# Performance work log

Hardware: AMD Instinct MI355X
Metric: run time of the kernel (lower is better)

Reference implementation:

```python
import jax, jax.numpy as jnp
import numpy as np

N_NODES = 50000
NEG_SLOPE_ATT = 0.2   # PyG GATConv default LeakyReLU slope for attention logits
NEG_SLOPE_ACT = 0.01  # nn.LeakyReLU default between layers


def _add_self_loops(src, dst, n):
    loop = jnp.arange(n, dtype=src.dtype)
    return jnp.concatenate([src, loop]), jnp.concatenate([dst, loop])


def gat_conv(x, W, a_src, a_dst, b, src, dst, n):
    # x: [N, Cin], W: [Cin, Cout], a_src/a_dst: [Cout], b: [Cout]
    h = x @ W                                   # [N, Cout]
    alpha_src = h @ a_src                       # [N]
    alpha_dst = h @ a_dst                       # [N]
    e = jax.nn.leaky_relu(alpha_src[src] + alpha_dst[dst], NEG_SLOPE_ATT)  # [E]
    # segment softmax over incoming edges of each dst node
    m = jax.ops.segment_max(e, dst, num_segments=n)      # [N]
    ex = jnp.exp(e - m[dst])                              # [E]
    s = jax.ops.segment_sum(ex, dst, num_segments=n)      # [N] (>0: self-loops)
    alpha = ex / s[dst]                                   # [E]
    out = jax.ops.segment_sum(h[src] * alpha[:, None], dst, num_segments=n)
    return out + b


def setup_inputs() -> dict:
    key = jax.random.key(0)
    ks = jax.random.split(key, 20)
    n, e = N_NODES, 800000
    cin, h1, h2, cout = 64, 128, 64, 32
    d = {
        "x": jax.random.normal(ks[0], (n, cin), jnp.float32),
        "edge_index": jax.random.randint(ks[1], (2, e), 0, n, jnp.int64),
    }
    dims = [(cin, h1), (h1, h2), (h2, h1), (h1, cout)]
    for i, (ci, co) in enumerate(dims, 1):
        g = 1.0 / np.sqrt(ci)
        d[f"W{i}"] = jax.random.normal(ks[2 + 4 * i], (ci, co), jnp.float32) * g
        d[f"a{i}s"] = jax.random.normal(ks[3 + 4 * i], (co,), jnp.float32) * 0.1
        d[f"a{i}d"] = jax.random.normal(ks[4 + 4 * i], (co,), jnp.float32) * 0.1
        d[f"b{i}"] = jnp.zeros((co,), jnp.float32)
    return d


def reference(x, edge_index, W1, a1s, a1d, b1, W2, a2s, a2d, b2,
              W3, a3s, a3d, b3, W4, a4s, a4d, b4):
    n = x.shape[0]
    src, dst = _add_self_loops(edge_index[0], edge_index[1], n)
    act = lambda t: jax.nn.leaky_relu(t, NEG_SLOPE_ACT)
    h = act(gat_conv(x, W1, a1s, a1d, b1, src, dst, n))
    # dropout is identity at inference
    h = act(gat_conv(h, W2, a2s, a2d, b2, src, dst, n))
    h = act(gat_conv(h, W3, a3s, a3d, b3, src, dst, n))
    return gat_conv(h, W4, a4s, a4d, b4, src, dst, n)
```

## Files before the change

kernel.cpp:

```cpp
#include <hip/hip_runtime.h>
#include <hip/hip_fp16.h>

#define NEG_ATT 0.2f


__global__ __launch_bounds__(256) void setup_k(int* cnt, int N, int NB,
                                               const float* __restrict__ W1, const float* __restrict__ a1s,
                                               const float* __restrict__ a1d, const float* __restrict__ W3,
                                               const float* __restrict__ a3s, const float* __restrict__ a3d,
                                               float* __restrict__ wa ) {
    int b = blockIdx.x;
    if (b < NB) {
        int i = b * 256 + threadIdx.x;
        if (i < N) cnt[i] = 0;
    } else {
        int t = threadIdx.x;
        int ci = t & 63;
        int which = t >> 6;
        const float* W = (which < 2) ? W1 : W3;
        const float* a = (which == 0) ? a1s : (which == 1) ? a1d : (which == 2) ? a3s : a3d;
        float s = 0.f;
        for (int co = 0; co < 128; ++co) s += W[ci * 128 + co] * a[co];
        wa[t] = s;
    }
}


__global__ __launch_bounds__(256) void scatter_gemv_k(const int* __restrict__ src, const int* __restrict__ dst,
                                                      int* cnt, unsigned short* __restrict__ col,
                                                      int E, int step, int SB, int iters4,
                                                      const float* __restrict__ X,
                                                      const float* __restrict__ was, const float* __restrict__ wad,
                                                      float* __restrict__ as_, float* __restrict__ ad_,
                                                      __half* __restrict__ x16, int N) {
    if (blockIdx.x < SB) {
        int part = blockIdx.x & 7;
        int lo = part * step, hi = lo + step;
        int tg = (blockIdx.x >> 3) * 256 + threadIdx.x;
        int stride = (SB >> 3) * 256;
        const int4* dst4 = (const int4*)dst;
        int E4 = E >> 2;
        for (int it = 0; it < iters4; ++it) {
            int i4 = tg + it * stride;
            if (i4 < E4) {
                int4 d4 = dst4[i4];
                int base = i4 << 2;
                if (d4.x >= lo && d4.x < hi) { int s = atomicAdd(&cnt[d4.x], 1); col[(d4.x << 6) + s] = (unsigned short)src[base]; }
                if (d4.y >= lo && d4.y < hi) { int s = atomicAdd(&cnt[d4.y], 1); col[(d4.y << 6) + s] = (unsigned short)src[base + 1]; }
                if (d4.z >= lo && d4.z < hi) { int s = atomicAdd(&cnt[d4.z], 1); col[(d4.z << 6) + s] = (unsigned short)src[base + 2]; }
                if (d4.w >= lo && d4.w < hi) { int s = atomicAdd(&cnt[d4.w], 1); col[(d4.w << 6) + s] = (unsigned short)src[base + 3]; }
            }
        }
        for (int i = (E & ~3) + tg; i < E; i += stride) {
            int dd = dst[i];
            if (dd >= lo && dd < hi) { int s = atomicAdd(&cnt[dd], 1); col[(dd << 6) + s] = (unsigned short)src[i]; }
        }
    } else {
        int wid  = ((blockIdx.x - SB) * 256 + threadIdx.x) >> 6;
        int lane = threadIdx.x & 63;
        if (wid >= N) return;
        float xv = X[(size_t)wid * 64 + lane];
        x16[(size_t)wid * 64 + lane] = __float2half(xv);
        float s1 = xv * was[lane];
        float s2 = xv * wad[lane];
        #pragma unroll
        for (int off = 32; off; off >>= 1) {
            s1 += __shfl_xor(s1, off);
            s2 += __shfl_xor(s2, off);
        }
        if (lane == 0) { as_[wid] = s1; ad_[wid] = s2; }
    }
}


__global__ __launch_bounds__(256) void gemm_wide_k(const __half* __restrict__ X16, const float* __restrict__ W,
                                                   const float* __restrict__ bias, __half* __restrict__ H16, int N) {
    __shared__ float Xs[128][68];
    __shared__ float Ws[64][128];
    int tid  = threadIdx.x;
    int row0 = blockIdx.x * 128;

    for (int i = tid; i < 2048; i += 256)
        *(float4*)&((float*)Ws)[i * 4] = *(const float4*)&W[i * 4];
    for (int i = tid; i < 2048; i += 256) {
        int r = i >> 4, k4 = i & 15;
        int gr = row0 + r;
        float4 v = {0.f, 0.f, 0.f, 0.f};
        if (gr < N) {
            uint2 pk = *(const uint2*)&X16[(size_t)gr * 64 + k4 * 4];
            float2 f0 = __half22float2(*(__half2*)&pk.x);
            float2 f1 = __half22float2(*(__half2*)&pk.y);
            v = make_float4(f0.x, f0.y, f1.x, f1.y);
        }
        *(float4*)&Xs[r][k4 * 4] = v;
    }
    __syncthreads();

    int ct = tid & 15;
    int rt = tid >> 4;
    float acc[8][8] = {};
    for (int k = 0; k < 64; k += 4) {
        float4 w0a = *(float4*)&Ws[k][ct * 8],     w0b = *(float4*)&Ws[k][ct * 8 + 4];
        float4 w1a = *(float4*)&Ws[k + 1][ct * 8], w1b = *(float4*)&Ws[k + 1][ct * 8 + 4];
        float4 w2a = *(float4*)&Ws[k + 2][ct * 8], w2b = *(float4*)&Ws[k + 2][ct * 8 + 4];
        float4 w3a = *(float4*)&Ws[k + 3][ct * 8], w3b = *(float4*)&Ws[k + 3][ct * 8 + 4];
        #pragma unroll
        for (int i = 0; i < 8; ++i) {
            float4 xv = *(float4*)&Xs[rt + 16 * i][k];
            acc[i][0] += xv.x * w0a.x + xv.y * w1a.x + xv.z * w2a.x + xv.w * w3a.x;
            acc[i][1] += xv.x * w0a.y + xv.y * w1a.y + xv.z * w2a.y + xv.w * w3a.y;
            acc[i][2] += xv.x * w0a.z + xv.y * w1a.z + xv.z * w2a.z + xv.w * w3a.z;
            acc[i][3] += xv.x * w0a.w + xv.y * w1a.w + xv.z * w2a.w + xv.w * w3a.w;
            acc[i][4] += xv.x * w0b.x + xv.y * w1b.x + xv.z * w2b.x + xv.w * w3b.x;
            acc[i][5] += xv.x * w0b.y + xv.y * w1b.y + xv.z * w2b.y + xv.w * w3b.y;
            acc[i][6] += xv.x * w0b.z + xv.y * w1b.z + xv.z * w2b.z + xv.w * w3b.z;
            acc[i][7] += xv.x * w0b.w + xv.y * w1b.w + xv.z * w2b.w + xv.w * w3b.w;
        }
    }

    float bv[8];
    #pragma unroll
    for (int j = 0; j < 8; ++j) bv[j] = bias[ct * 8 + j];

    #pragma unroll
    for (int i = 0; i < 8; ++i) {
        int gr = row0 + rt + 16 * i;
        if (gr < N) {
            float o[8];
            #pragma unroll
            for (int j = 0; j < 8; ++j) {
                float v = acc[i][j] + bv[j];
                o[j] = v > 0.f ? v : 0.01f * v;
            }
            __half2 h0 = __floats2half2_rn(o[0], o[1]);
            __half2 h1 = __floats2half2_rn(o[2], o[3]);
            __half2 h2 = __floats2half2_rn(o[4], o[5]);
            __half2 h3 = __floats2half2_rn(o[6], o[7]);
            uint4 pk = { *(unsigned*)&h0, *(unsigned*)&h1, *(unsigned*)&h2, *(unsigned*)&h3 };
            *(uint4*)&H16[(size_t)gr * 128 + ct * 8] = pk;
        }
    }
}


template <int CIN, int COUT>
__global__ __launch_bounds__(256) void gemm_k(const __half* __restrict__ X16, const float* __restrict__ W,
                                              const float* __restrict__ a_s, const float* __restrict__ a_d,
                                              __half* __restrict__ Hh, float* __restrict__ as_,
                                              float* __restrict__ ad_, int N) {
    constexpr int RB  = (CIN == 128 && COUT == 64) ? 32 : 64;
    constexpr int NCT = COUT / 4;
    constexpr int NRT = 256 / NCT;
    constexpr int RT  = RB / NRT;
    constexpr int XP  = CIN + 4;
    __shared__ float Xs[RB][XP];
    __shared__ float Ws[CIN][COUT];
    int tid  = threadIdx.x;
    int row0 = blockIdx.x * RB;

    for (int i = tid; i < CIN * COUT / 4; i += 256)
        *(float4*)&((float*)Ws)[i * 4] = *(const float4*)&W[i * 4];
    for (int i = tid; i < RB * CIN / 4; i += 256) {
        int r = i / (CIN / 4), k4 = i % (CIN / 4);
        int gr = row0 + r;
        float4 v = {0.f, 0.f, 0.f, 0.f};
        if (gr < N) {
            uint2 pk = *(const uint2*)&X16[(size_t)gr * CIN + k4 * 4];
            float2 f0 = __half22float2(*(__half2*)&pk.x);
            float2 f1 = __half22float2(*(__half2*)&pk.y);
            v = make_float4(f0.x, f0.y, f1.x, f1.y);
        }
        *(float4*)&Xs[r][k4 * 4] = v;
    }
    __syncthreads();

    int ct = tid % NCT;
    int rt = tid / NCT;
    float acc[RT][4] = {};
    for (int k = 0; k < CIN; k += 4) {
        float4 w0 = *(float4*)&Ws[k][ct * 4];
        float4 w1 = *(float4*)&Ws[k + 1][ct * 4];
        float4 w2 = *(float4*)&Ws[k + 2][ct * 4];
        float4 w3 = *(float4*)&Ws[k + 3][ct * 4];
        #pragma unroll
        for (int i = 0; i < RT; ++i) {
            float4 xv = *(float4*)&Xs[rt + i * NRT][k];
            acc[i][0] += xv.x * w0.x + xv.y * w1.x + xv.z * w2.x + xv.w * w3.x;
            acc[i][1] += xv.x * w0.y + xv.y * w1.y + xv.z * w2.y + xv.w * w3.y;
            acc[i][2] += xv.x * w0.z + xv.y * w1.z + xv.z * w2.z + xv.w * w3.z;
            acc[i][3] += xv.x * w0.w + xv.y * w1.w + xv.z * w2.w + xv.w * w3.w;
        }
    }

    float asv[4], adv[4];
    #pragma unroll
    for (int j = 0; j < 4; ++j) { asv[j] = a_s[ct * 4 + j]; adv[j] = a_d[ct * 4 + j]; }

    #pragma unroll
    for (int i = 0; i < RT; ++i) {
        int gr = row0 + rt + i * NRT;
        float s1 = acc[i][0] * asv[0] + acc[i][1] * asv[1] + acc[i][2] * asv[2] + acc[i][3] * asv[3];
        float s2 = acc[i][0] * adv[0] + acc[i][1] * adv[1] + acc[i][2] * adv[2] + acc[i][3] * adv[3];
        #pragma unroll
        for (int off = 1; off < NCT; off <<= 1) {
            s1 += __shfl_xor(s1, off);
            s2 += __shfl_xor(s2, off);
        }
        if (gr < N) {
            __half2 p0 = __floats2half2_rn(acc[i][0], acc[i][1]);
            __half2 p1 = __floats2half2_rn(acc[i][2], acc[i][3]);
            uint2 pk = { *(unsigned*)&p0, *(unsigned*)&p1 };
            *(uint2*)&Hh[(size_t)gr * COUT + ct * 4] = pk;
            if (ct == 0) { as_[gr] = s1; ad_[gr] = s2; }
        }
    }
}


template <int C, int MODE>
__global__ __launch_bounds__(256) void agg_k(const __half* __restrict__ Hg, const float* __restrict__ as_,
                                             const float* __restrict__ ad_, const int* __restrict__ deg,
                                             const unsigned short* __restrict__ col, const float* __restrict__ bias,
                                             const float* __restrict__ was, const float* __restrict__ wad,
                                             float* __restrict__ outf, __half* __restrict__ outh,
                                             float* __restrict__ oas, float* __restrict__ oad, int N) {
    __shared__ int2 sw[4][64];
    int wid  = (blockIdx.x * 256 + threadIdx.x) >> 6;
    int lane = threadIdx.x & 63;
    int wvi  = threadIdx.x >> 6;
    if (wid >= N) return;
    float adi = ad_[wid];
    int dg = deg[wid];
    float a0 = 0.f, a1 = 0.f, b0 = 0.f, b1 = 0.f;
    const int sub  = lane >> 5, c32 = lane & 31;
    const int quad = lane >> 4, c16 = lane & 15;

    int s_l = 0; float w_l = 0.f;
    if (lane < dg) {
        s_l = col[(wid << 6) + lane];
        float e = as_[s_l] + adi;
        e = e > 0.f ? e : NEG_ATT * e;
        w_l = __expf(e);
    }
    sw[wvi][lane] = make_int2(s_l, __float_as_int(w_l));

    float es = as_[wid] + adi;
    es = es > 0.f ? es : NEG_ATT * es;
    float ws = __expf(es);
    float denom = w_l + ((lane == 0) ? ws : 0.f);
    if (C == 64) {
        if (!sub) {
            float2 f = __half22float2(*(const __half2*)&Hg[((size_t)wid << 6) + 2 * c32]);
            a0 += ws * f.x; a1 += ws * f.y;
        }
    } else {
        if (!quad) {
            float2 f = __half22float2(*(const __half2*)&Hg[((size_t)wid << 5) + 2 * c16]);
            a0 += ws * f.x; a1 += ws * f.y;
        }
    }

    auto g64 = [&](int j, auto NEhalf) {
        constexpr int M = decltype(NEhalf)::value;
        float2 hv[M]; float wv[M];
        #pragma unroll
        for (int u = 0; u < M; ++u) {
            int2 p = sw[wvi][j + 2 * u + sub];
            wv[u] = __int_as_float(p.y);
            hv[u] = __half22float2(*(const __half2*)&Hg[((size_t)p.x << 6) + 2 * c32]);
        }
        #pragma unroll
        for (int u = 0; u < M; ++u) {
            if (u & 1) { b0 += wv[u] * hv[u].x; b1 += wv[u] * hv[u].y; }
            else       { a0 += wv[u] * hv[u].x; a1 += wv[u] * hv[u].y; }
        }
    };
    auto g32 = [&](int j, auto NEq) {
        constexpr int M = decltype(NEq)::value;
        float2 hv[M]; float wv[M];
        #pragma unroll
        for (int u = 0; u < M; ++u) {
            int2 p = sw[wvi][j + 4 * u + quad];
            wv[u] = __int_as_float(p.y);
            hv[u] = __half22float2(*(const __half2*)&Hg[((size_t)p.x << 5) + 2 * c16]);
        }
        #pragma unroll
        for (int u = 0; u < M; ++u) {
            if (u & 1) { b0 += wv[u] * hv[u].x; b1 += wv[u] * hv[u].y; }
            else       { a0 += wv[u] * hv[u].x; a1 += wv[u] * hv[u].y; }
        }
    };

    if (C == 64) {
        if (dg <= 8)       g64(0, std::integral_constant<int, 4>{});
        else if (dg <= 16) g64(0, std::integral_constant<int, 8>{});
        else if (dg <= 32) g64(0, std::integral_constant<int, 16>{});
        else { g64(0, std::integral_constant<int, 16>{}); g64(32, std::integral_constant<int, 16>{}); }
    } else {
        if (dg <= 16)      g32(0, std::integral_constant<int, 4>{});
        else if (dg <= 32) g32(0, std::integral_constant<int, 8>{});
        else { g32(0, std::integral_constant<int, 8>{}); g32(32, std::integral_constant<int, 8>{}); }
    }

    float f0 = a0 + b0, f1 = a1 + b1;
    if (C == 32) { f0 += __shfl_xor(f0, 16); f1 += __shfl_xor(f1, 16); }
    f0 += __shfl_xor(f0, 32); f1 += __shfl_xor(f1, 32);
    #pragma unroll
    for (int off = 32; off; off >>= 1) denom += __shfl_xor(denom, off);

    float inv = 1.f / denom;
    float v0 = f0 * inv, v1 = f1 * inv;

    if (MODE == 0) {
        if (!sub) {
            __half2 p = __floats2half2_rn(v0, v1);
            *(__half2*)&outh[((size_t)wid << 6) + 2 * c32] = p;
        }
    } else if (MODE == 1) {
        float2 bb = *(const float2*)&bias[2 * c32];
        v0 += bb.x; v1 += bb.y;
        v0 = v0 > 0.f ? v0 : 0.01f * v0;
        v1 = v1 > 0.f ? v1 : 0.01f * v1;
        if (!sub) {
            __half2 p = __floats2half2_rn(v0, v1);
            *(__half2*)&outh[((size_t)wid << 6) + 2 * c32] = p;
        }
        float2 wsv = *(const float2*)&was[2 * c32];
        float2 wdv = *(const float2*)&wad[2 * c32];
        float s1 = v0 * wsv.x + v1 * wsv.y;
        float s2 = v0 * wdv.x + v1 * wdv.y;
        #pragma unroll
        for (int off = 16; off; off >>= 1) {
            s1 += __shfl_xor(s1, off);
            s2 += __shfl_xor(s2, off);
        }
        if (lane == 0) { oas[wid] = s1; oad[wid] = s2; }
    } else {
        if (!quad) {
            float2 bb = *(const float2*)&bias[2 * c16];
            float2 o = {v0 + bb.x, v1 + bb.y};
            *(float2*)&outf[((size_t)wid << 5) + 2 * c16] = o;
        }
    }
}


extern "C" void kernel_launch(void* const* d_in, const int* in_sizes, int n_in,
                              void* d_out, int out_size, void* d_ws, size_t ws_size,
                              hipStream_t stream) {
    const float* x  = (const float*)d_in[0];
    const int* ei   = (const int*)d_in[1];
    const float* W1 = (const float*)d_in[2];
    const float* a1s = (const float*)d_in[3];
    const float* a1d = (const float*)d_in[4];
    const float* b1  = (const float*)d_in[5];
    const float* W2 = (const float*)d_in[6];
    const float* a2s = (const float*)d_in[7];
    const float* a2d = (const float*)d_in[8];
    const float* b2  = (const float*)d_in[9];
    const float* W3 = (const float*)d_in[10];
    const float* a3s = (const float*)d_in[11];
    const float* a3d = (const float*)d_in[12];
    const float* b3  = (const float*)d_in[13];
    const float* W4 = (const float*)d_in[14];
    const float* a4s = (const float*)d_in[15];
    const float* a4d = (const float*)d_in[16];
    const float* b4  = (const float*)d_in[17];

    const int N = in_sizes[0] / 64;
    const int E = in_sizes[1] / 2;
    const int* src = ei;
    const int* dst = ei + E;

    float* asA  = (float*)d_ws;
    float* adA  = asA + N;
    float* asB  = adA + N;
    float* adB  = asB + N;
    float* wa   = adB + N;
    int* cnt    = (int*)(wa + 256);
    unsigned short* col = (unsigned short*)(cnt + N);
    __half* x16 = (__half*)(col + (size_t)N * 64);
    __half* g1  = x16 + (size_t)N * 64;
    __half* g2  = g1 + (size_t)N * 64;
    __half* g3  = g2 + (size_t)N * 64;
    __half* g4  = g3 + (size_t)N * 64;

    const int NB = (N + 255) / 256;
    const int STEP = (N + 7) / 8;
    const int SB = 2048;
    const int ITERS4 = ((E >> 2) + (SB / 8) * 256 - 1) / ((SB / 8) * 256);
    const int NWAVE = (N * 64 + 255) / 256;

    setup_k<<<NB + 1, 256, 0, stream>>>(cnt, N, NB, W1, a1s, a1d, W3, a3s, a3d, wa);
    float* wa1s = wa, *wa1d = wa + 64, *wa3s = wa + 128, *wa3d = wa + 192;

    scatter_gemv_k<<<SB + NWAVE, 256, 0, stream>>>(src, dst, cnt, col, E, STEP, SB, ITERS4,
                                                   x, wa1s, wa1d, asA, adA, x16, N);

    agg_k<64, 0><<<NWAVE, 256, 0, stream>>>(x16, asA, adA, cnt, col, nullptr, nullptr, nullptr,
                                            nullptr, g3, nullptr, nullptr, N);
    gemm_wide_k<<<(N + 127) / 128, 256, 0, stream>>>(g3, W1, b1, g4, N);

    gemm_k<128, 64><<<(N + 31) / 32, 256, 0, stream>>>(g4, W2, a2s, a2d, g1, asB, adB, N);
    agg_k<64, 1><<<NWAVE, 256, 0, stream>>>(g1, asB, adB, cnt, col, b2, wa3s, wa3d,
                                            nullptr, g2, asA, adA, N);

    agg_k<64, 0><<<NWAVE, 256, 0, stream>>>(g2, asA, adA, cnt, col, nullptr, nullptr, nullptr,
                                            nullptr, g3, nullptr, nullptr, N);
    gemm_wide_k<<<(N + 127) / 128, 256, 0, stream>>>(g3, W3, b3, g4, N);

    gemm_k<128, 32><<<(N + 63) / 64, 256, 0, stream>>>(g4, W4, a4s, a4d, g1, asB, adB, N);
    agg_k<32, 2><<<NWAVE, 256, 0, stream>>>(g1, asB, adB, cnt, col, b4, nullptr, nullptr,
                                            (float*)d_out, nullptr, nullptr, nullptr, N);
}
```

Baseline: 243.5 us.

## Replace partitioned edge scatter with two-pass bucket binning by destination range

```diff
diff --git a/kernel.cpp b/kernel.cpp
--- a/kernel.cpp
+++ b/kernel.cpp
@@ -2,9 +2,10 @@
 #include <hip/hip_fp16.h>
 
 #define NEG_ATT 0.2f
-
-
-__global__ __launch_bounds__(256) void setup_k(int* cnt, int N, int NB,
+#define BCAP 160000
+
+
+__global__ __launch_bounds__(256) void setup_k(int* cnt, int N, int NB, int* bucketCnt,
                                                const float* __restrict__ W1, const float* __restrict__ a1s,
                                                const float* __restrict__ a1d, const float* __restrict__ W3,
                                                const float* __restrict__ a3s, const float* __restrict__ a3d,
@@ -15,6 +16,7 @@
         if (i < N) cnt[i] = 0;
     } else {
         int t = threadIdx.x;
+        if (t < 8) bucketCnt[t] = 0;
         int ci = t & 63;
         int which = t >> 6;
         const float* W = (which < 2) ? W1 : W3;
@@ -26,37 +28,54 @@
 }
 
 
-__global__ __launch_bounds__(256) void scatter_gemv_k(const int* __restrict__ src, const int* __restrict__ dst,
-                                                      int* cnt, unsigned short* __restrict__ col,
-                                                      int E, int step, int SB, int iters4,
-                                                      const float* __restrict__ X,
-                                                      const float* __restrict__ was, const float* __restrict__ wad,
-                                                      float* __restrict__ as_, float* __restrict__ ad_,
-                                                      __half* __restrict__ x16, int N) {
-    if (blockIdx.x < SB) {
-        int part = blockIdx.x & 7;
-        int lo = part * step, hi = lo + step;
-        int tg = (blockIdx.x >> 3) * 256 + threadIdx.x;
-        int stride = (SB >> 3) * 256;
-        const int4* dst4 = (const int4*)dst;
+__global__ __launch_bounds__(256) void binA_gemv_k(const int* __restrict__ src, const int* __restrict__ dst,
+                                                   unsigned* __restrict__ bucket, int* bucketCnt,
+                                                   int E, int step, int AB,
+                                                   const float* __restrict__ X,
+                                                   const float* __restrict__ was, const float* __restrict__ wad,
+                                                   float* __restrict__ as_, float* __restrict__ ad_,
+                                                   __half* __restrict__ x16, int N) {
+    if (blockIdx.x < AB) {
+        __shared__ int lcnt[8];
+        __shared__ int gbase[8];
+        int tid = threadIdx.x;
+        if (tid < 8) lcnt[tid] = 0;
+        __syncthreads();
+        int i4 = blockIdx.x * 256 + tid;
         int E4 = E >> 2;
-        for (int it = 0; it < iters4; ++it) {
-            int i4 = tg + it * stride;
-            if (i4 < E4) {
-                int4 d4 = dst4[i4];
-                int base = i4 << 2;
-                if (d4.x >= lo && d4.x < hi) { int s = atomicAdd(&cnt[d4.x], 1); col[(d4.x << 6) + s] = (unsigned short)src[base]; }
-                if (d4.y >= lo && d4.y < hi) { int s = atomicAdd(&cnt[d4.y], 1); col[(d4.y << 6) + s] = (unsigned short)src[base + 1]; }
-                if (d4.z >= lo && d4.z < hi) { int s = atomicAdd(&cnt[d4.z], 1); col[(d4.z << 6) + s] = (unsigned short)src[base + 2]; }
-                if (d4.w >= lo && d4.w < hi) { int s = atomicAdd(&cnt[d4.w], 1); col[(d4.w << 6) + s] = (unsigned short)src[base + 3]; }
+        bool va = i4 < E4;
+        int pp[4], loff[4];
+        unsigned pk[4];
+        if (va) {
+            int4 d4 = *(const int4*)&dst[i4 * 4];
+            int4 s4 = *(const int4*)&src[i4 * 4];
+            int dd[4] = {d4.x, d4.y, d4.z, d4.w};
+            int ss[4] = {s4.x, s4.y, s4.z, s4.w};
+            #pragma unroll
+            for (int u = 0; u < 4; ++u) {
+                int p = dd[u] / step;
+                pk[u] = ((unsigned)dd[u] << 16) | (unsigned)ss[u];
+                pp[u] = p;
+                loff[u] = atomicAdd(&lcnt[p], 1);
             }
         }
-        for (int i = (E & ~3) + tg; i < E; i += stride) {
+        __syncthreads();
+        if (tid < 8) gbase[tid] = atomicAdd(&bucketCnt[tid], lcnt[tid]);
+        __syncthreads();
+        if (va) {
+            #pragma unroll
+            for (int u = 0; u < 4; ++u)
+                bucket[pp[u] * BCAP + gbase[pp[u]] + loff[u]] = pk[u];
+        }
+        if (blockIdx.x == 0 && tid < (E & 3)) {
+            int i = (E & ~3) + tid;
             int dd = dst[i];
-            if (dd >= lo && dd < hi) { int s = atomicAdd(&cnt[dd], 1); col[(dd << 6) + s] = (unsigned short)src[i]; }
+            int p = dd / step;
+            int off = atomicAdd(&bucketCnt[p], 1);
+            bucket[p * BCAP + off] = ((unsigned)dd << 16) | (unsigned)src[i];
         }
     } else {
-        int wid  = ((blockIdx.x - SB) * 256 + threadIdx.x) >> 6;
+        int wid  = ((blockIdx.x - AB) * 256 + threadIdx.x) >> 6;
         int lane = threadIdx.x & 63;
         if (wid >= N) return;
         float xv = X[(size_t)wid * 64 + lane];
@@ -69,6 +88,22 @@
             s2 += __shfl_xor(s2, off);
         }
         if (lane == 0) { as_[wid] = s1; ad_[wid] = s2; }
+    }
+}
+
+
+__global__ __launch_bounds__(256) void binB_k(const unsigned* __restrict__ bucket, const int* __restrict__ bucketCnt,
+                                              int* cnt, unsigned short* __restrict__ col, int GB) {
+    int p = blockIdx.x & 7;
+    int n = bucketCnt[p];
+    int tg = (blockIdx.x >> 3) * 256 + threadIdx.x;
+    int stride = (GB >> 3) * 256;
+    for (int i = tg; i < n; i += stride) {
+        unsigned e = bucket[p * BCAP + i];
+        int dd = e >> 16;
+        unsigned short ss = (unsigned short)(e & 0xffff);
+        int slot = atomicAdd(&cnt[dd], 1);
+        col[(dd << 6) + slot] = ss;
     }
 }
 
@@ -377,9 +412,11 @@
     float* asB  = adA + N;
     float* adB  = asB + N;
     float* wa   = adB + N;
-    int* cnt    = (int*)(wa + 256);
+    int* bucketCnt = (int*)(wa + 256);
+    int* cnt    = bucketCnt + 16;
     unsigned short* col = (unsigned short*)(cnt + N);
-    __half* x16 = (__half*)(col + (size_t)N * 64);
+    unsigned* bucket = (unsigned*)(col + (size_t)N * 64);
+    __half* x16 = (__half*)(bucket + 8 * (size_t)BCAP);
     __half* g1  = x16 + (size_t)N * 64;
     __half* g2  = g1 + (size_t)N * 64;
     __half* g3  = g2 + (size_t)N * 64;
@@ -387,15 +424,17 @@
 
     const int NB = (N + 255) / 256;
     const int STEP = (N + 7) / 8;
-    const int SB = 2048;
-    const int ITERS4 = ((E >> 2) + (SB / 8) * 256 - 1) / ((SB / 8) * 256);
+    const int AB = ((E >> 2) + 255) / 256;
+    const int GB = 2048;
     const int NWAVE = (N * 64 + 255) / 256;
 
-    setup_k<<<NB + 1, 256, 0, stream>>>(cnt, N, NB, W1, a1s, a1d, W3, a3s, a3d, wa);
+    setup_k<<<NB + 1, 256, 0, stream>>>(cnt, N, NB, bucketCnt, W1, a1s, a1d, W3, a3s, a3d, wa);
     float* wa1s = wa, *wa1d = wa + 64, *wa3s = wa + 128, *wa3d = wa + 192;
 
-    scatter_gemv_k<<<SB + NWAVE, 256, 0, stream>>>(src, dst, cnt, col, E, STEP, SB, ITERS4,
-                                                   x, wa1s, wa1d, asA, adA, x16, N);
+    binA_gemv_k<<<AB + NWAVE, 256, 0, stream>>>(src, dst, bucket, bucketCnt, E, STEP, AB,
+                                                x, wa1s, wa1d, asA, adA, x16, N);
+
+    binB_k<<<GB, 256, 0, stream>>>(bucket, bucketCnt, cnt, col, GB);
 
     agg_k<64, 0><<<NWAVE, 256, 0, stream>>>(x16, asA, adA, cnt, col, nullptr, nullptr, nullptr,
                                             nullptr, g3, nullptr, nullptr, N);
```

Result: no change. 248.1 us (+1.9%).
